# Kernel tuning notes

Hardware: AMD Instinct MI355X
Metric: run time of the kernel (lower is better)

The kernel has to match this reference:

```python
import jax, jax.numpy as jnp
import numpy as np
import math

B, T, C, H = 8, 1024, 768, 12
HD = C // H  # 64


def setup_inputs() -> dict:
    key = jax.random.key(0)
    k1, k2, k3 = jax.random.split(key, 3)
    x = jax.random.normal(k1, (B, T, C), dtype=jnp.float32)
    W_attn = jax.random.normal(k2, (C, 3 * C), dtype=jnp.float32) * 0.02
    b_attn = jnp.zeros((3 * C,), dtype=jnp.float32)
    W_proj = jax.random.normal(k3, (C, C), dtype=jnp.float32) * (0.02 / math.sqrt(2 * 12))
    b_proj = jnp.zeros((C,), dtype=jnp.float32)
    return {"x": x, "W_attn": W_attn, "b_attn": b_attn, "W_proj": W_proj, "b_proj": b_proj}


def reference(x, W_attn, b_attn, W_proj, b_proj):
    Bx, Tx, Cx = x.shape
    qkv = x @ W_attn + b_attn                        # [B,T,3C]
    # faithful to original: reshape to (B,T,H,3*HD) then split last axis
    qkv = qkv.reshape(Bx, Tx, H, 3 * HD).transpose(0, 2, 1, 3)  # [B,H,T,3*HD]
    q, k, v = jnp.split(qkv, 3, axis=-1)             # each [B,H,T,HD]
    att = jnp.einsum('bhqd,bhkd->bhqk', q, k) / math.sqrt(HD)
    causal = jnp.tril(jnp.ones((Tx, Tx), dtype=bool))
    att = jnp.where(causal, att, -jnp.inf)
    att = jax.nn.softmax(att, axis=-1)
    y = jnp.einsum('bhqk,bhkd->bhqd', att, v)        # [B,H,T,HD]
    y = y.transpose(0, 2, 1, 3).reshape(Bx, Tx, Cx)  # [B,T,C]
    return y @ W_proj + b_proj
```

## Files before the change

kernel.cpp:

```cpp
#include <hip/hip_runtime.h>
#include <hip/hip_bf16.h>


#define TDIM 1024
#define CDIM 768
#define NDIM 2304

typedef __attribute__((ext_vector_type(8))) short bf16x8;
typedef __attribute__((ext_vector_type(8))) unsigned short u16x8;
typedef __attribute__((ext_vector_type(4))) float f32x4;

__device__ __forceinline__ unsigned short f2bf(float f) {
    unsigned int u;
    __builtin_memcpy(&u, &f, 4);
    u += 0x7FFFu + ((u >> 16) & 1u);
    return (unsigned short)(u >> 16);
}

__device__ __forceinline__ void async_copy16(void* lds, const void* g) {
    __builtin_amdgcn_global_load_lds(
        (const __attribute__((address_space(1))) void*)g,
        (__attribute__((address_space(3))) void*)lds, 16, 0, 0);
}

__global__ __launch_bounds__(256) void cast_x(const float* __restrict__ x,
                                              unsigned short* __restrict__ xb) {
    const size_t i = ((size_t)blockIdx.x * 256 + threadIdx.x) * 4;
    float4 v = *(const float4*)&x[i];
    ushort4 s;
    s.x = f2bf(v.x); s.y = f2bf(v.y); s.z = f2bf(v.z); s.w = f2bf(v.w);
    *(ushort4*)&xb[i] = s;
}

template <int N>
__global__ __launch_bounds__(256) void transpose_cast(const float* __restrict__ W,
                                                      unsigned short* __restrict__ Wt) {
    __shared__ float tile[32][33];
    const int n0 = blockIdx.x * 32;
    const int k0 = blockIdx.y * 32;
    const int tx = threadIdx.x & 31;
    const int ty = threadIdx.x >> 5;
#pragma unroll
    for (int i = 0; i < 4; ++i)
        tile[ty + i * 8][tx] = W[(size_t)(k0 + ty + i * 8) * N + n0 + tx];
    __syncthreads();
#pragma unroll
    for (int i = 0; i < 4; ++i)
        Wt[(size_t)(n0 + ty + i * 8) * CDIM + k0 + tx] = f2bf(tile[tx][ty + i * 8]);
}

__global__ __launch_bounds__(512, 4) void qkv_mfma(
    const unsigned short* __restrict__ xb, const unsigned short* __restrict__ Wt,
    const float* __restrict__ bias,
    unsigned short* __restrict__ Q, unsigned short* __restrict__ Kd,
    unsigned short* __restrict__ Vt)
{
    const int wg = ((int)blockIdx.x & 7) * 72 + ((int)blockIdx.x >> 3);
    const int bx = wg % 9;
    const int by = wg / 9;
    const int n0 = bx * 256;
    const int m0 = by * 128;
    const int tid = threadIdx.x;
    const int lane = tid & 63;
    const int w = tid >> 6;
    const int wm = w >> 2;
    const int wn = w & 3;
    const int lm = lane & 15;
    const int lq = lane >> 4;

    __shared__ __align__(16) unsigned short lds[36864];

    float bb[4];
#pragma unroll
    for (int ni = 0; ni < 4; ++ni) bb[ni] = bias[n0 + wn * 64 + ni * 16 + lm];

    f32x4 acc[4][4] = {};

    const int eo = lq ^ ((lm >> 1) & 3);
    int aoffc[4], boffc[4];
#pragma unroll
    for (int mi = 0; mi < 4; ++mi)
        aoffc[mi] = (wm * 64 + mi * 16 + lm) * 32 + eo * 8;
#pragma unroll
    for (int ni = 0; ni < 4; ++ni)
        boffc[ni] = 4096 + (wn * 64 + ni * 16 + lm) * 32 + eo * 8;

    const int rowA = tid >> 2;
    const int ccA = (tid & 3) ^ ((rowA >> 1) & 3);
    const int srcA = rowA * CDIM + ccA * 8;
    int srcB[2];
#pragma unroll
    for (int j = 0; j < 2; ++j) {
        const int lin = j * 512 + tid;
        const int rowB = lin >> 2;
        const int ccB = (lin & 3) ^ ((rowB >> 1) & 3);
        srcB[j] = rowB * CDIM + ccB * 8;
    }
    const unsigned short* xbb = xb + (size_t)m0 * CDIM;
    const unsigned short* Wtb = Wt + (size_t)n0 * CDIM;

#define STAGE(p, kt)                                                            \
    do {                                                                        \
        async_copy16(&lds[(p) * 12288 + w * 512], &xbb[srcA + (kt) * 32]);      \
        _Pragma("unroll")                                                       \
        for (int j = 0; j < 2; ++j)                                             \
            async_copy16(&lds[(p) * 12288 + 4096 + j * 4096 + w * 512],         \
                         &Wtb[srcB[j] + (kt) * 32]);                            \
    } while (0)

#define TILE(p, ktn)                                                            \
    do {                                                                        \
        STAGE((p + 2) % 3, ktn);                                                \
        bf16x8 a[4], b[4];                                                      \
        _Pragma("unroll")                                                       \
        for (int mi = 0; mi < 4; ++mi)                                          \
            a[mi] = *(const bf16x8*)&lds[(p) * 12288 + aoffc[mi]];              \
        _Pragma("unroll")                                                       \
        for (int ni = 0; ni < 4; ++ni)                                          \
            b[ni] = *(const bf16x8*)&lds[(p) * 12288 + boffc[ni]];              \
        __builtin_amdgcn_s_setprio(1);                                          \
        _Pragma("unroll")                                                       \
        for (int mi = 0; mi < 4; ++mi)                                          \
            _Pragma("unroll")                                                   \
            for (int ni = 0; ni < 4; ++ni)                                      \
                acc[mi][ni] = __builtin_amdgcn_mfma_f32_16x16x32_bf16(          \
                    a[mi], b[ni], acc[mi][ni], 0, 0, 0);                        \
        __builtin_amdgcn_s_setprio(0);                                          \
        asm volatile("s_waitcnt vmcnt(3)" ::: "memory");                        \
        __builtin_amdgcn_s_barrier();                                           \
    } while (0)

    STAGE(0, 0);
    STAGE(1, 1);
    asm volatile("s_waitcnt vmcnt(3)" ::: "memory");
    __builtin_amdgcn_s_barrier();

#pragma unroll 1
    for (int it = 0; it < 8; ++it) {
        const int k2 = (3 * it + 2 < 24) ? 3 * it + 2 : 23;
        const int k3 = (3 * it + 3 < 24) ? 3 * it + 3 : 23;
        const int k4 = (3 * it + 4 < 24) ? 3 * it + 4 : 23;
        TILE(0, k2);
        TILE(1, k3);
        TILE(2, k4);
    }

#undef STAGE
#undef TILE

    asm volatile("s_waitcnt vmcnt(0)" ::: "memory");
    __builtin_amdgcn_s_barrier();

    const int ga = bx * 4 + wn;
    const int which = ga % 3;
    const int h = ga / 3;

    if (which == 2) {
#pragma unroll
        for (int ni = 0; ni < 4; ++ni) {
            const int d = ni * 16 + lm;
#pragma unroll
            for (int mi = 0; mi < 4; ++mi) {
                const int gm0 = m0 + wm * 64 + mi * 16 + lq * 4;
                const int bidx = gm0 >> 10;
                const int t0 = gm0 & 1023;
                ushort4 sv;
                sv.x = f2bf(acc[mi][ni][0] + bb[ni]);
                sv.y = f2bf(acc[mi][ni][1] + bb[ni]);
                sv.z = f2bf(acc[mi][ni][2] + bb[ni]);
                sv.w = f2bf(acc[mi][ni][3] + bb[ni]);
                *(ushort4*)&Vt[(((size_t)bidx * 12 + h) * 64 + d) * TDIM + t0] = sv;
            }
        }
    } else {
        unsigned short* dst = (which == 0) ? Q : Kd;
        unsigned short* Es = &lds[w * 1152];
        const int erow = lane >> 2;
        const int ecol = lane & 3;
#pragma unroll
        for (int mi = 0; mi < 4; ++mi) {
#pragma unroll
            for (int r = 0; r < 4; ++r)
#pragma unroll
                for (int ni = 0; ni < 4; ++ni)
                    Es[(lq * 4 + r) * 72 + ni * 16 + lm] = f2bf(acc[mi][ni][r] + bb[ni]);
            const int t = m0 + wm * 64 + mi * 16 + erow;
            const int bidx = t >> 10;
            const int tt = t & 1023;
            unsigned short* drow = &dst[(((size_t)bidx * 12 + h) * TDIM + tt) * 64];
            u16x8 v0 = *(const u16x8*)&Es[erow * 72 + ecol * 16];
            u16x8 v1 = *(const u16x8*)&Es[erow * 72 + ecol * 16 + 8];
            *(u16x8*)&drow[ecol * 16] = v0;
            *(u16x8*)&drow[ecol * 16 + 8] = v1;
        }
    }
}

#define ATTN_TILE(aq, q0t, qt_t, l_p, o) do {                                   \
    const bool diag_ = (kt == (qt_t));                                          \
    float pf[4][4];                                                             \
    _Pragma("unroll")                                                           \
    for (int nt = 0; nt < 4; ++nt) {                                            \
        f32x4 s = {};                                                           \
        _Pragma("unroll")                                                       \
        for (int kc = 0; kc < 2; ++kc) {                                        \
            bf16x8 bfrag = *(const bf16x8*)&Ks[nt * 16 + lm][kc * 32 + lq * 8]; \
            s = __builtin_amdgcn_mfma_f32_16x16x32_bf16(aq[kc], bfrag, s, 0, 0, 0); \
        }                                                                       \
        const int keyg = kbase + nt * 16 + lm;                                  \
        _Pragma("unroll")                                                       \
        for (int r = 0; r < 4; ++r) {                                           \
            float p = __builtin_amdgcn_exp2f(s[r] * SC);                        \
            if (diag_) {                                                        \
                const int qg = (q0t) + w * 16 + lq * 4 + r;                     \
                if (keyg > qg) p = 0.f;                                         \
            }                                                                   \
            pf[nt][r] = p;                                                      \
        }                                                                       \
    }                                                                           \
    _Pragma("unroll")                                                           \
    for (int r = 0; r < 4; ++r) {                                               \
        l_p[r] += pf[0][r] + pf[1][r] + pf[2][r] + pf[3][r];                    \
        _Pragma("unroll")                                                       \
        for (int nt = 0; nt < 4; ++nt)                                          \
            Ps[w][lq * 4 + r][nt * 16 + lm] = f2bf(pf[nt][r]);                  \
    }                                                                           \
    {                                                                           \
        bf16x8 ap[2];                                                           \
        _Pragma("unroll")                                                       \
        for (int kc = 0; kc < 2; ++kc)                                          \
            ap[kc] = *(const bf16x8*)&Ps[w][lm][kc * 32 + lq * 8];              \
        _Pragma("unroll")                                                       \
        for (int nt = 0; nt < 4; ++nt) {                                        \
            _Pragma("unroll")                                                   \
            for (int kc = 0; kc < 2; ++kc) {                                    \
                bf16x8 bv = *(const bf16x8*)&Vts[nt * 16 + lm][kc * 32 + lq * 8]; \
                o[nt] = __builtin_amdgcn_mfma_f32_16x16x32_bf16(ap[kc], bv, o[nt], 0, 0, 0); \
            }                                                                   \
        }                                                                       \
    }                                                                           \
} while (0)

#define ATTN_EPI(q0t, l_p, o) do {                                              \
    _Pragma("unroll")                                                           \
    for (int r = 0; r < 4; ++r) {                                               \
        float l = l_p[r];                                                       \
        _Pragma("unroll")                                                       \
        for (int off = 1; off < 16; off <<= 1) l += __shfl_xor(l, off);         \
        const float inv = 1.0f / l;                                             \
        const int qg = (q0t) + w * 16 + lq * 4 + r;                             \
        _Pragma("unroll")                                                       \
        for (int nt = 0; nt < 4; ++nt)                                          \
            Yb[(size_t)qg * 64 + nt * 16 + lm] = f2bf(o[nt][r] * inv);          \
    }                                                                           \
} while (0)

__global__ __launch_bounds__(256) void attn_mfma(
    const unsigned short* __restrict__ Q, const unsigned short* __restrict__ K,
    const unsigned short* __restrict__ Vt, unsigned short* __restrict__ Y)
{
    const int pi = blockIdx.x;
    const int bh = blockIdx.y;
    const int qtA = pi, qtB = 15 - pi;
    const int q0A = qtA * 64, q0B = qtB * 64;
    const int tid = threadIdx.x;
    const int lane = tid & 63;
    const int w = tid >> 6;
    const int lm = lane & 15;
    const int lq = lane >> 4;

    __shared__ __align__(16) unsigned short Ks[64][72];
    __shared__ __align__(16) unsigned short Vts[64][72];
    __shared__ __align__(16) unsigned short Ps[4][16][72];

    const unsigned short* Qb = Q + (size_t)bh * TDIM * 64;
    const unsigned short* Kb = K + (size_t)bh * TDIM * 64;
    const unsigned short* Vtb = Vt + (size_t)bh * 64 * TDIM;
    unsigned short* Yb = Y + (size_t)bh * TDIM * 64;

    bf16x8 aqA[2], aqB[2];
#pragma unroll
    for (int kc = 0; kc < 2; ++kc) {
        aqA[kc] = *(const bf16x8*)&Qb[(size_t)(q0A + w * 16 + lm) * 64 + kc * 32 + lq * 8];
        aqB[kc] = *(const bf16x8*)&Qb[(size_t)(q0B + w * 16 + lm) * 64 + kc * 32 + lq * 8];
    }

    float lA[4] = {}, lB[4] = {};
    f32x4 oA[4] = {}, oB[4] = {};

    const float SC = 0.125f * 1.44269504f;
    const int nktA = qtA + 1;
    const int nktB = qtB + 1;

    for (int kt = 0; kt < nktB; ++kt) {
        const int kbase = kt * 64;
        __syncthreads();
#pragma unroll
        for (int it = 0; it < 2; ++it) {
            const int idx = tid + it * 256;
            const int r = idx >> 3;
            const int c = idx & 7;
            *(u16x8*)&Ks[r][c * 8] =
                *(const u16x8*)&Kb[(size_t)(kbase + r) * 64 + c * 8];
            *(u16x8*)&Vts[r][c * 8] =
                *(const u16x8*)&Vtb[(size_t)r * TDIM + kbase + c * 8];
        }
        __syncthreads();

        ATTN_TILE(aqB, q0B, qtB, lB, oB);
        if (kt < nktA) ATTN_TILE(aqA, q0A, qtA, lA, oA);
    }

    ATTN_EPI(q0A, lA, oA);
    ATTN_EPI(q0B, lB, oB);
}

__global__ __launch_bounds__(256) void proj_mfma(
    const unsigned short* __restrict__ Y, const unsigned short* __restrict__ Wt,
    const float* __restrict__ bias, float* __restrict__ out)
{
    const int n0 = blockIdx.x * 128;
    const int m0 = blockIdx.y * 128;
    const int tid = threadIdx.x;
    const int lane = tid & 63;
    const int w = tid >> 6;
    const int wm = w & 1;
    const int wn = w >> 1;
    const int lm = lane & 15;
    const int lq = lane >> 4;

    __shared__ __align__(16) unsigned short As[128 * 32];
    __shared__ __align__(16) unsigned short Bs[128 * 32];

    f32x4 acc[4][4] = {};

    const int srow = lane >> 2;
    const int schunk = lane & 3;

    for (int k0 = 0; k0 < CDIM; k0 += 32) {
        const int h = k0 >> 6;
        const int inner = k0 & 63;
        __syncthreads();
#pragma unroll
        for (int c = 0; c < 2; ++c) {
            const int rbase = c * 64 + w * 16;
            const int m = m0 + rbase + srow;
            const int bidx = m >> 10;
            const int t = m & 1023;
            async_copy16(&As[rbase * 32],
                         &Y[(((size_t)bidx * 12 + h) * TDIM + t) * 64 + inner + schunk * 8]);
            async_copy16(&Bs[rbase * 32],
                         &Wt[(size_t)(n0 + rbase + srow) * CDIM + k0 + schunk * 8]);
        }
        __syncthreads();

        bf16x8 a[4], b[4];
#pragma unroll
        for (int mi = 0; mi < 4; ++mi)
            a[mi] = *(const bf16x8*)&As[(wm * 64 + mi * 16 + lm) * 32 + lq * 8];
#pragma unroll
        for (int ni = 0; ni < 4; ++ni)
            b[ni] = *(const bf16x8*)&Bs[(wn * 64 + ni * 16 + lm) * 32 + lq * 8];
#pragma unroll
        for (int mi = 0; mi < 4; ++mi)
#pragma unroll
            for (int ni = 0; ni < 4; ++ni)
                acc[mi][ni] = __builtin_amdgcn_mfma_f32_16x16x32_bf16(
                    a[mi], b[ni], acc[mi][ni], 0, 0, 0);
    }

#pragma unroll
    for (int ni = 0; ni < 4; ++ni) {
        const int gn = n0 + wn * 64 + ni * 16 + lm;
        const float bb = bias[gn];
#pragma unroll
        for (int mi = 0; mi < 4; ++mi) {
#pragma unroll
            for (int r = 0; r < 4; ++r) {
                const int gm = m0 + wm * 64 + mi * 16 + lq * 4 + r;
                out[(size_t)gm * CDIM + gn] = acc[mi][ni][r] + bb;
            }
        }
    }
}

extern "C" void kernel_launch(void* const* d_in, const int* in_sizes, int n_in,
                              void* d_out, int out_size, void* d_ws, size_t ws_size,
                              hipStream_t stream) {
    const float* x      = (const float*)d_in[0];
    const float* W_attn = (const float*)d_in[1];
    const float* b_attn = (const float*)d_in[2];
    const float* W_proj = (const float*)d_in[3];
    const float* b_proj = (const float*)d_in[4];
    float* out = (float*)d_out;

    const size_t per = (size_t)8 * 12 * 1024 * 64;
    unsigned short* Q   = (unsigned short*)d_ws;
    unsigned short* K   = Q + per;
    unsigned short* Vt  = K + per;
    unsigned short* xb  = Vt + per;
    unsigned short* Wta = xb + (size_t)8192 * CDIM;
    unsigned short* Wtp = Wta + (size_t)NDIM * CDIM;

    cast_x<<<dim3(6144), 256, 0, stream>>>(x, xb);
    transpose_cast<NDIM><<<dim3(72, 24), 256, 0, stream>>>(W_attn, Wta);
    transpose_cast<CDIM><<<dim3(24, 24), 256, 0, stream>>>(W_proj, Wtp);

    qkv_mfma<<<dim3(576), 512, 0, stream>>>(xb, Wta, b_attn, Q, K, Vt);
    attn_mfma<<<dim3(8, 96), 256, 0, stream>>>(Q, K, Vt, Q);
    proj_mfma<<<dim3(6, 64), 256, 0, stream>>>(Q, Wtp, b_proj, out);
}
```

Measured before the change: 187.4 us.

## Double-buffer K/V tiles in attention with async global-to-LDS loads and XOR swizzle

The attention kernel now loads each K and V^T tile straight into LDS with async global_load_lds copies into two buffers. The next tile is prefetched while the current one is computed, which replaces the old load, sync, compute sequence and its two barriers per tile. The padded LDS rows are replaced with an XOR-swizzled layout so the MFMA fragment reads avoid bank conflicts without padding. The cost is double the K/V LDS footprint, which can lower occupancy, plus a full vmcnt wait and a barrier at the end of each tile.

Measured after the change: 187.5 us. No clear change (+0.1%).

```diff
diff --git a/kernel.cpp b/kernel.cpp
--- a/kernel.cpp
+++ b/kernel.cpp
@@ -196,7 +196,7 @@
     }
 }
 
-#define ATTN_TILE(aq, q0t, qt_t, l_p, o) do {                                   \
+#define ATTN_TILE(aq, q0t, qt_t, l_p, o, ksb, vsb) do {                         \
     const bool diag_ = (kt == (qt_t));                                          \
     float pf[4][4];                                                             \
     _Pragma("unroll")                                                           \
@@ -204,7 +204,7 @@
         f32x4 s = {};                                                           \
         _Pragma("unroll")                                                       \
         for (int kc = 0; kc < 2; ++kc) {                                        \
-            bf16x8 bfrag = *(const bf16x8*)&Ks[nt * 16 + lm][kc * 32 + lq * 8]; \
+            bf16x8 bfrag = *(const bf16x8*)&(ksb)[(nt * 16 + lm) * 64 + cofs[kc]]; \
             s = __builtin_amdgcn_mfma_f32_16x16x32_bf16(aq[kc], bfrag, s, 0, 0, 0); \
         }                                                                       \
         const int keyg = kbase + nt * 16 + lm;                                  \
@@ -234,7 +234,7 @@
         for (int nt = 0; nt < 4; ++nt) {                                        \
             _Pragma("unroll")                                                   \
             for (int kc = 0; kc < 2; ++kc) {                                    \
-                bf16x8 bv = *(const bf16x8*)&Vts[nt * 16 + lm][kc * 32 + lq * 8]; \
+                bf16x8 bv = *(const bf16x8*)&(vsb)[(nt * 16 + lm) * 64 + cofs[kc]]; \
                 o[nt] = __builtin_amdgcn_mfma_f32_16x16x32_bf16(ap[kc], bv, o[nt], 0, 0, 0); \
             }                                                                   \
         }                                                                       \
@@ -269,8 +269,8 @@
     const int lm = lane & 15;
     const int lq = lane >> 4;
 
-    __shared__ __align__(16) unsigned short Ks[64][72];
-    __shared__ __align__(16) unsigned short Vts[64][72];
+    __shared__ __align__(16) unsigned short Ks2[2][4096];
+    __shared__ __align__(16) unsigned short Vts2[2][4096];
     __shared__ __align__(16) unsigned short Ps[4][16][72];
 
     const unsigned short* Qb = Q + (size_t)bh * TDIM * 64;
@@ -285,6 +285,30 @@
         aqB[kc] = *(const bf16x8*)&Qb[(size_t)(q0B + w * 16 + lm) * 64 + kc * 32 + lq * 8];
     }
 
+    int dstO[2], srcK[2], srcV[2];
+#pragma unroll
+    for (int it = 0; it < 2; ++it) {
+        const int idx = it * 256 + tid;
+        const int row = idx >> 3;
+        const int cc = (idx & 7) ^ (row & 7);
+        dstO[it] = idx * 8;
+        srcK[it] = row * 64 + cc * 8;
+        srcV[it] = row * TDIM + cc * 8;
+    }
+    int cofs[2];
+#pragma unroll
+    for (int kc = 0; kc < 2; ++kc)
+        cofs[kc] = (((kc * 4 + lq) ^ (lm & 7)) * 8);
+
+#define AST(bf, kb)                                                             \
+    do {                                                                        \
+        _Pragma("unroll")                                                       \
+        for (int it = 0; it < 2; ++it) {                                        \
+            async_copy16(&Ks2[bf][dstO[it]], &Kb[(size_t)(kb) * 64 + srcK[it]]); \
+            async_copy16(&Vts2[bf][dstO[it]], &Vtb[(size_t)(kb) + srcV[it]]);   \
+        }                                                                       \
+    } while (0)
+
     float lA[4] = {}, lB[4] = {};
     f32x4 oA[4] = {}, oB[4] = {};
 
@@ -292,24 +316,24 @@
     const int nktA = qtA + 1;
     const int nktB = qtB + 1;
 
+    int buf = 0;
+    AST(0, 0);
+    asm volatile("s_waitcnt vmcnt(0)" ::: "memory");
+    __builtin_amdgcn_s_barrier();
+
     for (int kt = 0; kt < nktB; ++kt) {
         const int kbase = kt * 64;
-        __syncthreads();
-#pragma unroll
-        for (int it = 0; it < 2; ++it) {
-            const int idx = tid + it * 256;
-            const int r = idx >> 3;
-            const int c = idx & 7;
-            *(u16x8*)&Ks[r][c * 8] =
-                *(const u16x8*)&Kb[(size_t)(kbase + r) * 64 + c * 8];
-            *(u16x8*)&Vts[r][c * 8] =
-                *(const u16x8*)&Vtb[(size_t)r * TDIM + kbase + c * 8];
-        }
-        __syncthreads();
-
-        ATTN_TILE(aqB, q0B, qtB, lB, oB);
-        if (kt < nktA) ATTN_TILE(aqA, q0A, qtA, lA, oA);
-    }
+        if (kt + 1 < nktB) AST(buf ^ 1, kbase + 64);
+
+        ATTN_TILE(aqB, q0B, qtB, lB, oB, Ks2[buf], Vts2[buf]);
+        if (kt < nktA) ATTN_TILE(aqA, q0A, qtA, lA, oA, Ks2[buf], Vts2[buf]);
+
+        asm volatile("s_waitcnt vmcnt(0)" ::: "memory");
+        __builtin_amdgcn_s_barrier();
+        buf ^= 1;
+    }
+
+#undef AST
 
     ATTN_EPI(q0A, lA, oA);
     ATTN_EPI(q0B, lB, oB);
```
